# Performance work log

Hardware: AMD Instinct MI355X
Metric: run time of the kernel (lower is better)

## Reference

```python
import jax, jax.numpy as jnp
import numpy as np

D = 512
H = 8
W = 128  # window_size
HD = D // H
EPS = 1e-5


def _layernorm(x, g, b):
    mu = jnp.mean(x, axis=-1, keepdims=True)
    var = jnp.mean(jnp.square(x - mu), axis=-1, keepdims=True)
    return (x - mu) * jax.lax.rsqrt(var + EPS) * g + b


def setup_inputs() -> dict:
    key = jax.random.key(0)
    ks = jax.random.split(key, 6)
    B, S = 4, 8192
    src = jax.random.normal(ks[0], (B, S, D), jnp.float32)
    sc = 1.0 / np.sqrt(D)
    in_proj_w = jax.random.normal(ks[1], (3 * D, D), jnp.float32) * sc
    in_proj_b = jnp.zeros((3 * D,), jnp.float32)
    out_w = jax.random.normal(ks[2], (D, D), jnp.float32) * sc
    out_b = jnp.zeros((D,), jnp.float32)
    w1 = jax.random.normal(ks[3], (4 * D, D), jnp.float32) * sc
    b1 = jnp.zeros((4 * D,), jnp.float32)
    w2 = jax.random.normal(ks[4], (D, 4 * D), jnp.float32) * (1.0 / np.sqrt(4 * D))
    b2 = jnp.zeros((D,), jnp.float32)
    return {
        'src': src,
        'in_proj_w': in_proj_w, 'in_proj_b': in_proj_b,
        'out_w': out_w, 'out_b': out_b,
        'ln1_g': jnp.ones((D,), jnp.float32), 'ln1_b': jnp.zeros((D,), jnp.float32),
        'w1': w1, 'b1': b1, 'w2': w2, 'b2': b2,
        'ln2_g': jnp.ones((D,), jnp.float32), 'ln2_b': jnp.zeros((D,), jnp.float32),
    }


def reference(src, in_proj_w, in_proj_b, out_w, out_b, ln1_g, ln1_b,
              w1, b1, w2, b2, ln2_g, ln2_b):
    B, S, _ = src.shape
    nW = S // W
    x = src.reshape(B, nW, W, D)  # block-diagonal windows
    # packed qkv projection (torch MultiheadAttention in_proj)
    qkv = jnp.einsum('bnwd,ed->bnwe', x, in_proj_w) + in_proj_b
    q, k, v = jnp.split(qkv, 3, axis=-1)
    q = q.reshape(B, nW, W, H, HD)
    k = k.reshape(B, nW, W, H, HD)
    v = v.reshape(B, nW, W, H, HD)
    scores = jnp.einsum('bnqhd,bnkhd->bnhqk', q, k) / np.sqrt(HD)
    probs = jax.nn.softmax(scores, axis=-1)
    attn = jnp.einsum('bnhqk,bnkhd->bnqhd', probs, v).reshape(B, nW, W, D)
    attn = jnp.einsum('bnwd,ed->bnwe', attn, out_w) + out_b
    x = _layernorm(x + attn, ln1_g, ln1_b)
    ff = jnp.einsum('bnwf,df->bnwd', jax.nn.relu(jnp.einsum('bnwd,fd->bnwf', x, w1) + b1), w2) + b2
    x = _layernorm(x + ff, ln2_g, ln2_b)
    return x.reshape(B, S, D)
```

## Files before the change

### kernel.cpp

```cpp
#include <hip/hip_runtime.h>
#include <hip/hip_bf16.h>
#include <math.h>

typedef __bf16 bf16;
typedef bf16 bf16x8 __attribute__((ext_vector_type(8)));
typedef bf16 bf16x4 __attribute__((ext_vector_type(4)));
typedef float f32x4 __attribute__((ext_vector_type(4)));

#define MFMA16(a, b, c) __builtin_amdgcn_mfma_f32_16x16x32_bf16(a, b, c, 0, 0, 0)

__device__ __forceinline__ uint32_t swz(uint32_t base, uint32_t row, uint32_t rs, uint32_t cb) {
    return base + row * rs + (((cb >> 4) ^ (row & 7u)) << 4) + (cb & 15u);
}

__device__ __forceinline__ void gload16(const void* g, void* l) {
    __builtin_amdgcn_global_load_lds((const __attribute__((address_space(1))) void*)g,
                                     (__attribute__((address_space(3))) void*)l, 16, 0, 0);
}



__global__ void wcvt_kernel(const float* __restrict__ wqkv, const float* __restrict__ wout,
                            const float* __restrict__ w1f, const float* __restrict__ w2f,
                            bf16* __restrict__ o) {
    int i = blockIdx.x * blockDim.x + threadIdx.x;
    const float* s;
    int soff, doff;
    if (i < 98304) {
        int u = i;
        int tile = u >> 10, c = (u >> 8) & 3, nn = u & 255;
        int n = (tile >> 4) * 256 + nn;
        int k = (tile & 15) * 32 + c * 8;
        s = wqkv; soff = n * 512 + k; doff = u * 8;
    } else if (i < 131072) {
        int u = i - 98304;
        int tile = u >> 11, c = (u >> 9) & 3, nn = u & 511;
        int k = tile * 32 + c * 8;
        s = wout; soff = nn * 512 + k; doff = 786432 + u * 8;
    } else if (i < 262144) {
        int u = i - 131072;
        int tile = u >> 10, c = (u >> 8) & 3, nn = u & 255;
        int n = (tile >> 4) * 256 + nn;
        int k = (tile & 15) * 32 + c * 8;
        s = w1f; soff = n * 512 + k; doff = 1048576 + u * 8;
    } else {
        int u = i - 262144;
        int tile = u >> 10, c = (u >> 8) & 3, nn = u & 255;
        int n = (tile >> 6) * 256 + nn;
        int k = (tile & 63) * 32 + c * 8;
        s = w2f; soff = n * 2048 + k; doff = 2097152 + u * 8;
    }
    float4 v0 = *(const float4*)(s + soff);
    float4 v1 = *(const float4*)(s + soff + 4);
    bf16x8 h = { (bf16)v0.x, (bf16)v0.y, (bf16)v0.z, (bf16)v0.w,
                 (bf16)v1.x, (bf16)v1.y, (bf16)v1.z, (bf16)v1.w };
    *(bf16x8*)(o + doff) = h;
}

__global__ void xcvt_kernel(float* __restrict__ src) {
    int row = blockIdx.x * 4 + (threadIdx.x >> 6);
    int l = threadIdx.x & 63;
    float* rp = src + (size_t)row * 512 + l * 8;
    float4 v0 = *(const float4*)rp;
    float4 v1 = *(const float4*)(rp + 4);
    asm volatile("s_waitcnt vmcnt(0)" ::: "memory");
    bf16x8 h = { (bf16)v0.x, (bf16)v0.y, (bf16)v0.z, (bf16)v0.w,
                 (bf16)v1.x, (bf16)v1.y, (bf16)v1.z, (bf16)v1.w };
    *(bf16x8*)((bf16*)(src + (size_t)row * 512) + l * 8) = h;
}

#define N256_LOOP(NT)                                                                  \
    int ib = 0;                                                                        \
    _Pragma("unroll 1")                                                                \
    for (int t = 0; t < (NT); ++t) {                                                   \
        int in2 = ib + 2; if (in2 >= 3) in2 -= 3;                                      \
        const uint32_t A0 = (uint32_t)ib * 8192u;                                      \
        const uint32_t B0 = 24576u + (uint32_t)ib * 16384u;                            \
        bf16x8 a[4], b[4];                                                             \
        _Pragma("unroll")                                                              \
        for (int i = 0; i < 4; ++i)                                                    \
            a[i] = *(const bf16x8*)(smem + A0 + quad * 2048 + (wm * 64 + i * 16 + l16) * 16); \
        _Pragma("unroll")                                                              \
        for (int nt = 0; nt < 4; ++nt)                                                 \
            b[nt] = *(const bf16x8*)(smem + B0 + quad * 4096 + (wn * 64 + nt * 16 + l16) * 16); \
        if (t + 2 < (NT)) { STAGE_A(in2, t + 2); STAGE_B2(in2, t + 2, 0); STAGE_B2(in2, t + 2, 1); } \
        _Pragma("unroll")                                                              \
        for (int nt = 0; nt < 4; ++nt)                                                 \
            _Pragma("unroll")                                                          \
            for (int i = 0; i < 4; ++i) acc[i][nt] = MFMA16(a[i], b[nt], acc[i][nt]);  \
        if (t + 2 < (NT)) asm volatile("s_waitcnt vmcnt(3)" ::: "memory");             \
        else              asm volatile("s_waitcnt vmcnt(0)" ::: "memory");             \
        __builtin_amdgcn_s_barrier();                                                  \
        ib = (ib == 2) ? 0 : ib + 1;                                                   \
    }

#define PHASED_LOOP(NT)                                                                \
    int ib = 0;                                                                        \
    _Pragma("unroll 1")                                                                \
    for (int t = 0; t < (NT); ++t) {                                                   \
        int in2 = ib + 2; if (in2 >= 3) in2 -= 3;                                      \
        const uint32_t A0 = (uint32_t)ib * 8192u;                                      \
        const uint32_t B0 = 24576u + (uint32_t)ib * 32768u;                            \
        bf16x8 a[4], b[8];                                                             \
                                                                \
        _Pragma("unroll")                                                              \
        for (int i = 0; i < 4; ++i)                                                    \
            a[i] = *(const bf16x8*)(smem + A0 + quad * 2048 + (wm * 64 + i * 16 + l16) * 16); \
        _Pragma("unroll")                                                              \
        for (int nt = 0; nt < 4; ++nt)                                                 \
            b[nt] = *(const bf16x8*)(smem + B0 + quad * 8192 + (wn * 128 + nt * 16 + l16) * 16); \
        if (t + 2 < (NT)) { STAGE_A(in2, t + 2); STAGE_B(in2, t + 2, 0); }             \
        __builtin_amdgcn_s_barrier();                                                  \
        asm volatile("s_waitcnt lgkmcnt(0)" ::: "memory");                             \
        __builtin_amdgcn_sched_barrier(0);                                             \
        __builtin_amdgcn_s_setprio(1);                                                 \
        _Pragma("unroll")                                                              \
        for (int nt = 0; nt < 4; ++nt)                                                 \
            _Pragma("unroll")                                                          \
            for (int i = 0; i < 4; ++i) acc[i][nt] = MFMA16(a[i], b[nt], acc[i][nt]);  \
        __builtin_amdgcn_s_setprio(0);                                                 \
        __builtin_amdgcn_s_barrier();                                                  \
                                                                \
        _Pragma("unroll")                                                              \
        for (int nt = 4; nt < 8; ++nt)                                                 \
            b[nt] = *(const bf16x8*)(smem + B0 + quad * 8192 + (wn * 128 + nt * 16 + l16) * 16); \
        if (t + 2 < (NT)) { STAGE_B(in2, t + 2, 1); STAGE_B(in2, t + 2, 2); STAGE_B(in2, t + 2, 3); } \
        __builtin_amdgcn_s_barrier();                                                  \
        asm volatile("s_waitcnt lgkmcnt(0)" ::: "memory");                             \
        __builtin_amdgcn_sched_barrier(0);                                             \
        __builtin_amdgcn_s_setprio(1);                                                 \
        _Pragma("unroll")                                                              \
        for (int nt = 4; nt < 8; ++nt)                                                 \
            _Pragma("unroll")                                                          \
            for (int i = 0; i < 4; ++i) acc[i][nt] = MFMA16(a[i], b[nt], acc[i][nt]);  \
        __builtin_amdgcn_s_setprio(0);                                                 \
        if (t + 2 < (NT)) asm volatile("s_waitcnt vmcnt(5)" ::: "memory");             \
        else              asm volatile("s_waitcnt vmcnt(0)" ::: "memory");             \
        __builtin_amdgcn_s_barrier();                                                  \
        ib = (ib == 2) ? 0 : ib + 1;                                                   \
    }

extern "C" __global__ __launch_bounds__(512, 4)
void qkv_kernel(const char* __restrict__ xb, const char* __restrict__ Wqkvp,
                const float* __restrict__ bqkv, char* __restrict__ qOb,
                char* __restrict__ kvb) {
    extern __shared__ char smem[];
    const int tid = threadIdx.x;
    const int w = tid >> 6, lane = tid & 63, l16 = lane & 15, quad = lane >> 4;
    const int wm = w >> 2, wn = w & 3;
    const int mb = blockIdx.x, cb = blockIdx.y;

    f32x4 acc[4][4];
#pragma unroll
    for (int i = 0; i < 4; ++i)
#pragma unroll
        for (int nt = 0; nt < 4; ++nt) acc[i][nt] = (f32x4){0.f, 0.f, 0.f, 0.f};

#define STAGE_A(ib_, t_)                                                               \
    {                                                                                  \
        int ca = w >> 1, rg = w & 1;                                                   \
        gload16(xb + (size_t)(mb * 128 + rg * 64 + lane) * 2048 + (t_) * 64 + ca * 16, \
                smem + (uint32_t)(ib_) * 8192u + ca * 2048 + rg * 1024);               \
    }
#define STAGE_B2(ib_, t_, j_)                                                          \
    {                                                                                  \
        int idx = w * 2 + (j_), c = idx >> 2, ng = idx & 3;                            \
        gload16(Wqkvp + (size_t)(cb * 16 + (t_)) * 16384 + c * 4096 + ng * 1024 + lane * 16, \
                smem + 24576u + (uint32_t)(ib_) * 16384u + (uint32_t)c * 4096 + (uint32_t)ng * 1024); \
    }

    STAGE_A(0, 0); STAGE_B2(0, 0, 0); STAGE_B2(0, 0, 1);
    STAGE_A(1, 1); STAGE_B2(1, 1, 0); STAGE_B2(1, 1, 1);
    asm volatile("s_waitcnt vmcnt(3)" ::: "memory");
    __builtin_amdgcn_s_barrier();

    N256_LOOP(16)
#undef STAGE_A
#undef STAGE_B2

    const uint32_t sb = 24576u + (uint32_t)w * 2048u;
#pragma unroll
    for (int i = 0; i < 4; ++i) {
#pragma unroll
        for (int nt = 0; nt < 4; ++nt) {
            float bb = bqkv[cb * 256 + wn * 64 + nt * 16 + l16];
#pragma unroll
            for (int r = 0; r < 4; ++r)
                *(bf16*)(smem + swz(sb, quad * 4 + r, 128, (nt * 16 + l16) * 2)) =
                    (bf16)(acc[i][nt][r] + bb);
        }
        asm volatile("s_waitcnt lgkmcnt(0)" ::: "memory");
#pragma unroll
        for (int t2 = 0; t2 < 2; ++t2) {
            int row = t2 * 8 + (lane >> 3), ch = lane & 7;
            bf16x8 v = *(bf16x8*)(smem + swz(sb, row, 128, ch * 16));
            size_t row_g = (size_t)(mb * 128 + wm * 64 + i * 16 + row);
            int cbyte = wn * 128 + ch * 16;
            if (cb < 2)      *(bf16x8*)(qOb + row_g * 1024 + cb * 512 + cbyte) = v;
            else if (cb < 4) *(bf16x8*)(kvb + row_g * 2048 + (cb - 2) * 512 + cbyte) = v;
            else             *(bf16x8*)(kvb + row_g * 2048 + 1024 + (cb - 4) * 512 + cbyte) = v;
        }
        asm volatile("s_waitcnt lgkmcnt(0)" ::: "memory");
    }
}

#define AVT 0u
#define ASCR 16384u
extern "C" __global__ __launch_bounds__(512, 4)
void attn_kernel(char* __restrict__ qOb, const char* __restrict__ kvb) {
    extern __shared__ char smem[];
    const int tid = threadIdx.x;
    const int wid = tid >> 6, lane = tid & 63, l16 = lane & 15, quad = lane >> 4;
    const int win = blockIdx.x >> 3, head = blockIdx.x & 7;
    const size_t wrow0 = (size_t)win * 128;
    f32x4 zero4 = { 0.f, 0.f, 0.f, 0.f };

    {
        int key = tid >> 2, d0 = (tid & 3) * 16;
        const char* vs = kvb + (wrow0 + key) * 2048 + 1024 + head * 128 + d0 * 2;
#pragma unroll
        for (int j = 0; j < 2; ++j) {
            bf16x8 v = *(const bf16x8*)(vs + j * 16);
#pragma unroll
            for (int e = 0; e < 8; ++e)
                *(bf16*)(smem + swz(AVT, d0 + j * 8 + e, 256, key * 2)) = v[e];
        }
    }
    __syncthreads();

    bf16x8 qf[2];
#pragma unroll
    for (int ks = 0; ks < 2; ++ks)
        qf[ks] = *(const bf16x8*)(qOb + (wrow0 + wid * 16 + l16) * 1024 + head * 128 + ks * 64 + quad * 16);

    f32x4 sa[8];
#pragma unroll
    for (int nt = 0; nt < 8; ++nt) sa[nt] = zero4;
#pragma unroll
    for (int nt = 0; nt < 8; ++nt)
#pragma unroll
        for (int ks = 0; ks < 2; ++ks) {
            bf16x8 kb = *(const bf16x8*)(kvb + (wrow0 + nt * 16 + l16) * 2048 + head * 128 + ks * 64 + quad * 16);
            sa[nt] = MFMA16(qf[ks], kb, sa[nt]);
        }
#pragma unroll
    for (int nt = 0; nt < 8; ++nt) sa[nt] *= 0.125f;
#pragma unroll
    for (int r = 0; r < 4; ++r) {
        float m = sa[0][r];
#pragma unroll
        for (int nt = 1; nt < 8; ++nt) m = fmaxf(m, sa[nt][r]);
#pragma unroll
        for (int sft = 1; sft < 16; sft <<= 1) m = fmaxf(m, __shfl_xor(m, sft, 64));
        float s = 0.f;
#pragma unroll
        for (int nt = 0; nt < 8; ++nt) {
            float e = __expf(sa[nt][r] - m);
            sa[nt][r] = e;
            s += e;
        }
#pragma unroll
        for (int sft = 1; sft < 16; sft <<= 1) s += __shfl_xor(s, sft, 64);
        float inv = 1.0f / s;
#pragma unroll
        for (int nt = 0; nt < 8; ++nt) sa[nt][r] *= inv;
    }

    const uint32_t sb = ASCR + (uint32_t)wid * 2048;
    bf16x8 pf[4];
#pragma unroll
    for (int hf = 0; hf < 2; ++hf) {
#pragma unroll
        for (int nt = 0; nt < 4; ++nt)
#pragma unroll
            for (int r = 0; r < 4; ++r)
                *(bf16*)(smem + swz(sb, quad * 4 + r, 128, (nt * 16 + l16) * 2)) = (bf16)sa[hf * 4 + nt][r];
        asm volatile("s_waitcnt lgkmcnt(0)" ::: "memory");
#pragma unroll
        for (int ks = 0; ks < 2; ++ks)
            pf[hf * 2 + ks] = *(bf16x8*)(smem + swz(sb, l16, 128, ks * 64 + quad * 16));
        asm volatile("s_waitcnt lgkmcnt(0)" ::: "memory");
    }

    f32x4 ov[4];
#pragma unroll
    for (int nt = 0; nt < 4; ++nt) {
        ov[nt] = zero4;
#pragma unroll
        for (int ks = 0; ks < 4; ++ks) {
            bf16x8 vb = *(bf16x8*)(smem + swz(AVT, nt * 16 + l16, 256, ks * 64 + quad * 16));
            ov[nt] = MFMA16(pf[ks], vb, ov[nt]);
        }
    }
#pragma unroll
    for (int hf = 0; hf < 2; ++hf) {
#pragma unroll
        for (int nt = 0; nt < 2; ++nt)
#pragma unroll
            for (int r = 0; r < 4; ++r)
                *(bf16*)(smem + swz(sb, quad * 4 + r, 128, (nt * 16 + l16) * 2)) = (bf16)ov[hf * 2 + nt][r];
        asm volatile("s_waitcnt lgkmcnt(0)" ::: "memory");
        {
            int row = lane >> 2, ch = lane & 3;
            bf16x8 v = *(bf16x8*)(smem + swz(sb, row, 128, ch * 16));
            *(bf16x8*)(qOb + (wrow0 + wid * 16 + row) * 1024 + head * 128 + hf * 64 + ch * 16) = v;
        }
        asm volatile("s_waitcnt lgkmcnt(0)" ::: "memory");
    }
}

extern "C" __global__ __launch_bounds__(512, 2)
void outproj_kernel(char* __restrict__ srcb, const char* __restrict__ qOb,
                    const char* __restrict__ Woutp, const float* __restrict__ bout,
                    const float* __restrict__ g1, const float* __restrict__ be1) {
    extern __shared__ char smem[];
    const int tid = threadIdx.x;
    const int w = tid >> 6, lane = tid & 63, l16 = lane & 15, quad = lane >> 4;
    const int wm = w >> 2, wn = w & 3;
    const int mb = blockIdx.x;

    f32x4 acc[4][8];
#pragma unroll
    for (int i = 0; i < 4; ++i)
#pragma unroll
        for (int nt = 0; nt < 8; ++nt) acc[i][nt] = (f32x4){0.f, 0.f, 0.f, 0.f};

#define STAGE_A(ib_, t_)                                                               \
    {                                                                                  \
        int ca = w >> 1, rg = w & 1;                                                   \
        gload16(qOb + (size_t)(mb * 128 + rg * 64 + lane) * 1024 + (t_) * 64 + ca * 16, \
                smem + (uint32_t)(ib_) * 8192u + ca * 2048 + rg * 1024);               \
    }
#define STAGE_B(ib_, t_, j_)                                                           \
    {                                                                                  \
        int idx = w * 4 + (j_), c = idx >> 3, ng = idx & 7;                            \
        gload16(Woutp + (size_t)(t_) * 32768 + c * 8192 + ng * 1024 + lane * 16,       \
                smem + 24576u + (uint32_t)(ib_) * 32768u + (uint32_t)c * 8192 + (uint32_t)ng * 1024); \
    }

    STAGE_A(0, 0); STAGE_B(0, 0, 0); STAGE_B(0, 0, 1); STAGE_B(0, 0, 2); STAGE_B(0, 0, 3);
    STAGE_A(1, 1); STAGE_B(1, 1, 0); STAGE_B(1, 1, 1); STAGE_B(1, 1, 2); STAGE_B(1, 1, 3);
    asm volatile("s_waitcnt vmcnt(5)" ::: "memory");
    __builtin_amdgcn_s_barrier();

    PHASED_LOOP(16)
#undef STAGE_A
#undef STAGE_B

#pragma unroll
    for (int nt = 0; nt < 8; ++nt) {
        int col = wn * 128 + nt * 16 + l16;
        float bb = bout[col];
#pragma unroll
        for (int i = 0; i < 4; ++i)
#pragma unroll
            for (int r = 0; r < 4; ++r) {
                int row = mb * 128 + wm * 64 + i * 16 + quad * 4 + r;
                float xv = (float)*(const bf16*)(srcb + (size_t)row * 2048 + col * 2);
                acc[i][nt][r] += bb + xv;
            }
    }
    float ps[4][4], ps2[4][4];
#pragma unroll
    for (int i = 0; i < 4; ++i)
#pragma unroll
        for (int r = 0; r < 4; ++r) {
            float s = 0.f, s2 = 0.f;
#pragma unroll
            for (int nt = 0; nt < 8; ++nt) {
                float v = acc[i][nt][r];
                s += v;
                s2 += v * v;
            }
#pragma unroll
            for (int sft = 1; sft < 16; sft <<= 1) {
                s += __shfl_xor(s, sft, 64);
                s2 += __shfl_xor(s2, sft, 64);
            }
            ps[i][r] = s;
            ps2[i][r] = s2;
        }
    if (l16 == 0) {
#pragma unroll
        for (int i = 0; i < 4; ++i)
#pragma unroll
            for (int r = 0; r < 4; ++r) {
                int row_l = wm * 64 + i * 16 + quad * 4 + r;
                *(float*)(smem + row_l * 32 + wn * 8) = ps[i][r];
                *(float*)(smem + row_l * 32 + wn * 8 + 4) = ps2[i][r];
            }
    }
    __syncthreads();
    const uint32_t sb = 24576u + (uint32_t)w * 4096u;
#pragma unroll
    for (int i = 0; i < 4; ++i) {
#pragma unroll
        for (int r = 0; r < 4; ++r) {
            int row_l = wm * 64 + i * 16 + quad * 4 + r;
            float S = 0.f, S2 = 0.f;
#pragma unroll
            for (int w4 = 0; w4 < 4; ++w4) {
                S += *(const float*)(smem + row_l * 32 + w4 * 8);
                S2 += *(const float*)(smem + row_l * 32 + w4 * 8 + 4);
            }
            float mu = S * (1.0f / 512.0f);
            float var = S2 * (1.0f / 512.0f) - mu * mu;
            float rstd = rsqrtf(var + 1e-5f);
#pragma unroll
            for (int nt = 0; nt < 8; ++nt) {
                int col = wn * 128 + nt * 16 + l16;
                float v = (acc[i][nt][r] - mu) * rstd * g1[col] + be1[col];
                *(bf16*)(smem + swz(sb, quad * 4 + r, 256, (nt * 16 + l16) * 2)) = (bf16)v;
            }
        }
        asm volatile("s_waitcnt lgkmcnt(0)" ::: "memory");
#pragma unroll
        for (int j = 0; j < 4; ++j) {
            int uu = j * 64 + lane;
            int row = uu >> 4, ch = uu & 15;
            bf16x8 v = *(bf16x8*)(smem + swz(sb, row, 256, ch * 16));
            *(bf16x8*)(srcb + (size_t)(mb * 128 + wm * 64 + i * 16 + row) * 2048 + 1024 +
                       wn * 256 + ch * 16) = v;
        }
        asm volatile("s_waitcnt lgkmcnt(0)" ::: "memory");
    }
}

extern "C" __global__ __launch_bounds__(512, 4)
void ff1_kernel(char* __restrict__ srcb, const char* __restrict__ W1p,
                const float* __restrict__ b1, char* __restrict__ doutb,
                char* __restrict__ wsOb) {
    extern __shared__ char smem[];
    const int tid = threadIdx.x;
    const int w = tid >> 6, lane = tid & 63, l16 = lane & 15, quad = lane >> 4;
    const int wm = w >> 2, wn = w & 3;
    const int mb = blockIdx.x, cb = blockIdx.y;

    f32x4 acc[4][4];
#pragma unroll
    for (int i = 0; i < 4; ++i)
#pragma unroll
        for (int nt = 0; nt < 4; ++nt) acc[i][nt] = (f32x4){0.f, 0.f, 0.f, 0.f};

#define STAGE_A(ib_, t_)                                                               \
    {                                                                                  \
        int ca = w >> 1, rg = w & 1;                                                   \
        gload16(srcb + (size_t)(mb * 128 + rg * 64 + lane) * 2048 + 1024 + (t_) * 64 + ca * 16, \
                smem + (uint32_t)(ib_) * 8192u + ca * 2048 + rg * 1024);               \
    }
#define STAGE_B2(ib_, t_, j_)                                                          \
    {                                                                                  \
        int idx = w * 2 + (j_), c = idx >> 2, ng = idx & 3;                            \
        gload16(W1p + (size_t)(cb * 16 + (t_)) * 16384 + c * 4096 + ng * 1024 + lane * 16, \
                smem + 24576u + (uint32_t)(ib_) * 16384u + (uint32_t)c * 4096 + (uint32_t)ng * 1024); \
    }

    STAGE_A(0, 0); STAGE_B2(0, 0, 0); STAGE_B2(0, 0, 1);
    STAGE_A(1, 1); STAGE_B2(1, 1, 0); STAGE_B2(1, 1, 1);
    asm volatile("s_waitcnt vmcnt(3)" ::: "memory");
    __builtin_amdgcn_s_barrier();

    N256_LOOP(16)
#undef STAGE_A
#undef STAGE_B2

    const uint32_t sb = 24576u + (uint32_t)w * 2048u;
#pragma unroll
    for (int i = 0; i < 4; ++i) {
#pragma unroll
        for (int nt = 0; nt < 4; ++nt) {
            float bb = b1[cb * 256 + wn * 64 + nt * 16 + l16];
#pragma unroll
            for (int r = 0; r < 4; ++r)
                *(bf16*)(smem + swz(sb, quad * 4 + r, 128, (nt * 16 + l16) * 2)) =
                    (bf16)fmaxf(acc[i][nt][r] + bb, 0.0f);
        }
        asm volatile("s_waitcnt lgkmcnt(0)" ::: "memory");
#pragma unroll
        for (int t2 = 0; t2 < 2; ++t2) {
            int row = t2 * 8 + (lane >> 3), ch = lane & 7;
            bf16x8 v = *(bf16x8*)(smem + swz(sb, row, 128, ch * 16));
            size_t row_g = (size_t)(mb * 128 + wm * 64 + i * 16 + row);
            int cbyte = wn * 128 + ch * 16;
            if (cb < 4)      *(bf16x8*)(doutb + row_g * 2048 + cb * 512 + cbyte) = v;
            else if (cb < 6) *(bf16x8*)(srcb + row_g * 2048 + (cb - 4) * 512 + cbyte) = v;
            else             *(bf16x8*)(wsOb + row_g * 1024 + (cb - 6) * 512 + cbyte) = v;
        }
        asm volatile("s_waitcnt lgkmcnt(0)" ::: "memory");
    }
}

extern "C" __global__ __launch_bounds__(512, 4)
void ff2_kernel(char* __restrict__ doutb, const char* __restrict__ srcb,
                const char* __restrict__ wsOb, const char* __restrict__ W2p,
                const float* __restrict__ b2) {
    extern __shared__ char smem[];
    const int tid = threadIdx.x;
    const int w = tid >> 6, lane = tid & 63, l16 = lane & 15, quad = lane >> 4;
    const int wm = w >> 2, wn = w & 3;
    const int mb = blockIdx.x, cb = blockIdx.y;

    f32x4 acc[4][4];
#pragma unroll
    for (int i = 0; i < 4; ++i)
#pragma unroll
        for (int nt = 0; nt < 4; ++nt) acc[i][nt] = (f32x4){0.f, 0.f, 0.f, 0.f};

#define STAGE_A(ib_, t_)                                                               \
    {                                                                                  \
        const char* hb; int rstride, koffb;                                            \
        if ((t_) < 32)      { hb = doutb; rstride = 2048; koffb = (t_) * 64; }         \
        else if ((t_) < 48) { hb = srcb;  rstride = 2048; koffb = ((t_) - 32) * 64; }  \
        else                { hb = wsOb;  rstride = 1024; koffb = ((t_) - 48) * 64; }  \
        int ca = w >> 1, rg = w & 1;                                                   \
        gload16(hb + (size_t)(mb * 128 + rg * 64 + lane) * rstride + koffb + ca * 16,  \
                smem + (uint32_t)(ib_) * 8192u + ca * 2048 + rg * 1024);               \
    }
#define STAGE_B2(ib_, t_, j_)                                                          \
    {                                                                                  \
        int idx = w * 2 + (j_), c = idx >> 2, ng = idx & 3;                            \
        gload16(W2p + (size_t)(cb * 64 + (t_)) * 16384 + c * 4096 + ng * 1024 + lane * 16, \
                smem + 24576u + (uint32_t)(ib_) * 16384u + (uint32_t)c * 4096 + (uint32_t)ng * 1024); \
    }

    STAGE_A(0, 0); STAGE_B2(0, 0, 0); STAGE_B2(0, 0, 1);
    STAGE_A(1, 1); STAGE_B2(1, 1, 0); STAGE_B2(1, 1, 1);
    asm volatile("s_waitcnt vmcnt(3)" ::: "memory");
    __builtin_amdgcn_s_barrier();

    N256_LOOP(64)
#undef STAGE_A
#undef STAGE_B2

#pragma unroll
    for (int nt = 0; nt < 4; ++nt) {
        int col = cb * 256 + wn * 64 + nt * 16 + l16;
        float bb = b2[col];
#pragma unroll
        for (int i = 0; i < 4; ++i)
#pragma unroll
            for (int r = 0; r < 4; ++r) {
                int row = mb * 128 + wm * 64 + i * 16 + quad * 4 + r;
                float x1v = (float)*(const bf16*)(srcb + (size_t)row * 2048 + 1024 + col * 2);
                *(float*)(doutb + (size_t)row * 2048 + col * 4) = acc[i][nt][r] + bb + x1v;
            }
    }
}

extern "C" __global__ __launch_bounds__(256)
void ln2_kernel(float* __restrict__ y, const float* __restrict__ g2,
                const float* __restrict__ be2) {
    int row = blockIdx.x * 4 + (threadIdx.x >> 6);
    int lane = threadIdx.x & 63;
    float* rp = y + (size_t)row * 512 + lane * 8;
    float4 v0 = *(const float4*)rp;
    float4 v1 = *(const float4*)(rp + 4);
    float s = v0.x + v0.y + v0.z + v0.w + v1.x + v1.y + v1.z + v1.w;
    float s2 = v0.x * v0.x + v0.y * v0.y + v0.z * v0.z + v0.w * v0.w +
               v1.x * v1.x + v1.y * v1.y + v1.z * v1.z + v1.w * v1.w;
#pragma unroll
    for (int sft = 1; sft < 64; sft <<= 1) {
        s += __shfl_xor(s, sft, 64);
        s2 += __shfl_xor(s2, sft, 64);
    }
    float mu = s * (1.0f / 512.0f);
    float var = s2 * (1.0f / 512.0f) - mu * mu;
    float rstd = rsqrtf(var + 1e-5f);
    const float* gp = g2 + lane * 8;
    const float* bp = be2 + lane * 8;
    float4 o0, o1;
    o0.x = (v0.x - mu) * rstd * gp[0] + bp[0];
    o0.y = (v0.y - mu) * rstd * gp[1] + bp[1];
    o0.z = (v0.z - mu) * rstd * gp[2] + bp[2];
    o0.w = (v0.w - mu) * rstd * gp[3] + bp[3];
    o1.x = (v1.x - mu) * rstd * gp[4] + bp[4];
    o1.y = (v1.y - mu) * rstd * gp[5] + bp[5];
    o1.z = (v1.z - mu) * rstd * gp[6] + bp[6];
    o1.w = (v1.w - mu) * rstd * gp[7] + bp[7];
    *(float4*)rp = o0;
    *(float4*)(rp + 4) = o1;
}

extern "C" void kernel_launch(void* const* d_in, const int* in_sizes, int n_in,
                              void* d_out, int out_size, void* d_ws, size_t ws_size,
                              hipStream_t stream) {
    (void)in_sizes; (void)n_in; (void)out_size; (void)ws_size;
    float* src = (float*)d_in[0];
    const float* ipw = (const float*)d_in[1];
    const float* ipb = (const float*)d_in[2];
    const float* ow  = (const float*)d_in[3];
    const float* ob  = (const float*)d_in[4];
    const float* g1  = (const float*)d_in[5];
    const float* be1 = (const float*)d_in[6];
    const float* w1  = (const float*)d_in[7];
    const float* b1  = (const float*)d_in[8];
    const float* w2  = (const float*)d_in[9];
    const float* b2  = (const float*)d_in[10];
    const float* g2  = (const float*)d_in[11];
    const float* be2 = (const float*)d_in[12];
    bf16* ws = (bf16*)d_ws;
    char* srcb = (char*)src;
    char* doutb = (char*)d_out;
    char* qOb = (char*)d_ws + 6291456;

    wcvt_kernel<<<1536, 256, 0, stream>>>(ipw, ow, w1, w2, ws);
    xcvt_kernel<<<8192, 256, 0, stream>>>(src);

    hipFuncSetAttribute((const void*)qkv_kernel, hipFuncAttributeMaxDynamicSharedMemorySize, 73728);
    hipFuncSetAttribute((const void*)attn_kernel, hipFuncAttributeMaxDynamicSharedMemorySize, 32768);
    hipFuncSetAttribute((const void*)outproj_kernel, hipFuncAttributeMaxDynamicSharedMemorySize, 122880);
    hipFuncSetAttribute((const void*)ff1_kernel, hipFuncAttributeMaxDynamicSharedMemorySize, 73728);
    hipFuncSetAttribute((const void*)ff2_kernel, hipFuncAttributeMaxDynamicSharedMemorySize, 73728);

    qkv_kernel<<<dim3(256, 6), 512, 73728, stream>>>(srcb, (const char*)ws, ipb, qOb, doutb);
    attn_kernel<<<2048, 512, 32768, stream>>>(qOb, doutb);
    outproj_kernel<<<256, 512, 122880, stream>>>(srcb, qOb, (const char*)(ws + 786432), ob, g1, be1);
    ff1_kernel<<<dim3(256, 8), 512, 73728, stream>>>(srcb, (const char*)(ws + 1048576), b1, doutb, qOb);
    ff2_kernel<<<dim3(256, 2), 512, 73728, stream>>>(doutb, srcb, qOb, (const char*)(ws + 2097152), b2);
    ln2_kernel<<<8192, 256, 0, stream>>>((float*)doutb, g2, be2);
}
```

Measured before the change: 488.6 us.

## Switch GEMMs to double-buffered LDS and split outproj with separate LN1 kernel

The shared GEMM loop goes from triple-buffered to double-buffered LDS, prefetching only one tile ahead and waiting on all loads each iteration. This cuts dynamic shared memory from 72KB to 48KB per block to allow more resident blocks. The out-projection is split over two 256-column blocks using the common N256 loop instead of the phased 512-wide loop, writing fp32 pre-norm output to a buffer. A new row-wise ln1_kernel then applies LayerNorm1, which adds a kernel launch and an extra fp32 round trip through global memory. The trade is less latency hiding in the main loop in exchange for higher occupancy and simpler code.

```diff
diff --git a/kernel.cpp b/kernel.cpp
--- a/kernel.cpp
+++ b/kernel.cpp
@@ -34,9 +34,10 @@
         s = wqkv; soff = n * 512 + k; doff = u * 8;
     } else if (i < 131072) {
         int u = i - 98304;
-        int tile = u >> 11, c = (u >> 9) & 3, nn = u & 511;
-        int k = tile * 32 + c * 8;
-        s = wout; soff = nn * 512 + k; doff = 786432 + u * 8;
+        int tile = u >> 10, c = (u >> 8) & 3, nn = u & 255;
+        int n = (tile >> 4) * 256 + nn;
+        int k = (tile & 15) * 32 + c * 8;
+        s = wout; soff = n * 512 + k; doff = 786432 + u * 8;
     } else if (i < 262144) {
         int u = i - 131072;
         int tile = u >> 10, c = (u >> 8) & 3, nn = u & 255;
@@ -73,9 +74,9 @@
     int ib = 0;                                                                        \
     _Pragma("unroll 1")                                                                \
     for (int t = 0; t < (NT); ++t) {                                                   \
-        int in2 = ib + 2; if (in2 >= 3) in2 -= 3;                                      \
+        if (t + 1 < (NT)) { STAGE_A(ib ^ 1, t + 1); STAGE_B2(ib ^ 1, t + 1, 0); STAGE_B2(ib ^ 1, t + 1, 1); } \
         const uint32_t A0 = (uint32_t)ib * 8192u;                                      \
-        const uint32_t B0 = 24576u + (uint32_t)ib * 16384u;                            \
+        const uint32_t B0 = 16384u + (uint32_t)ib * 16384u;                            \
         bf16x8 a[4], b[4];                                                             \
         _Pragma("unroll")                                                              \
         for (int i = 0; i < 4; ++i)                                                    \
@@ -83,61 +84,13 @@
         _Pragma("unroll")                                                              \
         for (int nt = 0; nt < 4; ++nt)                                                 \
             b[nt] = *(const bf16x8*)(smem + B0 + quad * 4096 + (wn * 64 + nt * 16 + l16) * 16); \
-        if (t + 2 < (NT)) { STAGE_A(in2, t + 2); STAGE_B2(in2, t + 2, 0); STAGE_B2(in2, t + 2, 1); } \
         _Pragma("unroll")                                                              \
         for (int nt = 0; nt < 4; ++nt)                                                 \
             _Pragma("unroll")                                                          \
             for (int i = 0; i < 4; ++i) acc[i][nt] = MFMA16(a[i], b[nt], acc[i][nt]);  \
-        if (t + 2 < (NT)) asm volatile("s_waitcnt vmcnt(3)" ::: "memory");             \
-        else              asm volatile("s_waitcnt vmcnt(0)" ::: "memory");             \
+        asm volatile("s_waitcnt vmcnt(0)" ::: "memory");                               \
         __builtin_amdgcn_s_barrier();                                                  \
-        ib = (ib == 2) ? 0 : ib + 1;                                                   \
-    }
-
-#define PHASED_LOOP(NT)                                                                \
-    int ib = 0;                                                                        \
-    _Pragma("unroll 1")                                                                \
-    for (int t = 0; t < (NT); ++t) {                                                   \
-        int in2 = ib + 2; if (in2 >= 3) in2 -= 3;                                      \
-        const uint32_t A0 = (uint32_t)ib * 8192u;                                      \
-        const uint32_t B0 = 24576u + (uint32_t)ib * 32768u;                            \
-        bf16x8 a[4], b[8];                                                             \
-                                                                \
-        _Pragma("unroll")                                                              \
-        for (int i = 0; i < 4; ++i)                                                    \
-            a[i] = *(const bf16x8*)(smem + A0 + quad * 2048 + (wm * 64 + i * 16 + l16) * 16); \
-        _Pragma("unroll")                                                              \
-        for (int nt = 0; nt < 4; ++nt)                                                 \
-            b[nt] = *(const bf16x8*)(smem + B0 + quad * 8192 + (wn * 128 + nt * 16 + l16) * 16); \
-        if (t + 2 < (NT)) { STAGE_A(in2, t + 2); STAGE_B(in2, t + 2, 0); }             \
-        __builtin_amdgcn_s_barrier();                                                  \
-        asm volatile("s_waitcnt lgkmcnt(0)" ::: "memory");                             \
-        __builtin_amdgcn_sched_barrier(0);                                             \
-        __builtin_amdgcn_s_setprio(1);                                                 \
-        _Pragma("unroll")                                                              \
-        for (int nt = 0; nt < 4; ++nt)                                                 \
-            _Pragma("unroll")                                                          \
-            for (int i = 0; i < 4; ++i) acc[i][nt] = MFMA16(a[i], b[nt], acc[i][nt]);  \
-        __builtin_amdgcn_s_setprio(0);                                                 \
-        __builtin_amdgcn_s_barrier();                                                  \
-                                                                \
-        _Pragma("unroll")                                                              \
-        for (int nt = 4; nt < 8; ++nt)                                                 \
-            b[nt] = *(const bf16x8*)(smem + B0 + quad * 8192 + (wn * 128 + nt * 16 + l16) * 16); \
-        if (t + 2 < (NT)) { STAGE_B(in2, t + 2, 1); STAGE_B(in2, t + 2, 2); STAGE_B(in2, t + 2, 3); } \
-        __builtin_amdgcn_s_barrier();                                                  \
-        asm volatile("s_waitcnt lgkmcnt(0)" ::: "memory");                             \
-        __builtin_amdgcn_sched_barrier(0);                                             \
-        __builtin_amdgcn_s_setprio(1);                                                 \
-        _Pragma("unroll")                                                              \
-        for (int nt = 4; nt < 8; ++nt)                                                 \
-            _Pragma("unroll")                                                          \
-            for (int i = 0; i < 4; ++i) acc[i][nt] = MFMA16(a[i], b[nt], acc[i][nt]);  \
-        __builtin_amdgcn_s_setprio(0);                                                 \
-        if (t + 2 < (NT)) asm volatile("s_waitcnt vmcnt(5)" ::: "memory");             \
-        else              asm volatile("s_waitcnt vmcnt(0)" ::: "memory");             \
-        __builtin_amdgcn_s_barrier();                                                  \
-        ib = (ib == 2) ? 0 : ib + 1;                                                   \
+        ib ^= 1;                                                                       \
     }
 
 extern "C" __global__ __launch_bounds__(512, 4)
@@ -166,19 +119,18 @@
     {                                                                                  \
         int idx = w * 2 + (j_), c = idx >> 2, ng = idx & 3;                            \
         gload16(Wqkvp + (size_t)(cb * 16 + (t_)) * 16384 + c * 4096 + ng * 1024 + lane * 16, \
-                smem + 24576u + (uint32_t)(ib_) * 16384u + (uint32_t)c * 4096 + (uint32_t)ng * 1024); \
+                smem + 16384u + (uint32_t)(ib_) * 16384u + (uint32_t)c * 4096 + (uint32_t)ng * 1024); \
     }
 
     STAGE_A(0, 0); STAGE_B2(0, 0, 0); STAGE_B2(0, 0, 1);
-    STAGE_A(1, 1); STAGE_B2(1, 1, 0); STAGE_B2(1, 1, 1);
-    asm volatile("s_waitcnt vmcnt(3)" ::: "memory");
+    asm volatile("s_waitcnt vmcnt(0)" ::: "memory");
     __builtin_amdgcn_s_barrier();
 
     N256_LOOP(16)
 #undef STAGE_A
 #undef STAGE_B2
 
-    const uint32_t sb = 24576u + (uint32_t)w * 2048u;
+    const uint32_t sb = 16384u + (uint32_t)w * 2048u;
 #pragma unroll
     for (int i = 0; i < 4; ++i) {
 #pragma unroll
@@ -309,21 +261,21 @@
     }
 }
 
-extern "C" __global__ __launch_bounds__(512, 2)
-void outproj_kernel(char* __restrict__ srcb, const char* __restrict__ qOb,
+extern "C" __global__ __launch_bounds__(512, 4)
+void outproj_kernel(const char* __restrict__ srcb, const char* __restrict__ qOb,
                     const char* __restrict__ Woutp, const float* __restrict__ bout,
-                    const float* __restrict__ g1, const float* __restrict__ be1) {
+                    char* __restrict__ doutb) {
     extern __shared__ char smem[];
     const int tid = threadIdx.x;
     const int w = tid >> 6, lane = tid & 63, l16 = lane & 15, quad = lane >> 4;
     const int wm = w >> 2, wn = w & 3;
-    const int mb = blockIdx.x;
-
-    f32x4 acc[4][8];
+    const int mb = blockIdx.x, cb = blockIdx.y;
+
+    f32x4 acc[4][4];
 #pragma unroll
     for (int i = 0; i < 4; ++i)
 #pragma unroll
-        for (int nt = 0; nt < 8; ++nt) acc[i][nt] = (f32x4){0.f, 0.f, 0.f, 0.f};
+        for (int nt = 0; nt < 4; ++nt) acc[i][nt] = (f32x4){0.f, 0.f, 0.f, 0.f};
 
 #define STAGE_A(ib_, t_)                                                               \
     {                                                                                  \
@@ -331,25 +283,24 @@
         gload16(qOb + (size_t)(mb * 128 + rg * 64 + lane) * 1024 + (t_) * 64 + ca * 16, \
                 smem + (uint32_t)(ib_) * 8192u + ca * 2048 + rg * 1024);               \
     }
-#define STAGE_B(ib_, t_, j_)                                                           \
-    {                                                                                  \
-        int idx = w * 4 + (j_), c = idx >> 3, ng = idx & 7;                            \
-        gload16(Woutp + (size_t)(t_) * 32768 + c * 8192 + ng * 1024 + lane * 16,       \
-                smem + 24576u + (uint32_t)(ib_) * 32768u + (uint32_t)c * 8192 + (uint32_t)ng * 1024); \
-    }
-
-    STAGE_A(0, 0); STAGE_B(0, 0, 0); STAGE_B(0, 0, 1); STAGE_B(0, 0, 2); STAGE_B(0, 0, 3);
-    STAGE_A(1, 1); STAGE_B(1, 1, 0); STAGE_B(1, 1, 1); STAGE_B(1, 1, 2); STAGE_B(1, 1, 3);
-    asm volatile("s_waitcnt vmcnt(5)" ::: "memory");
+#define STAGE_B2(ib_, t_, j_)                                                          \
+    {                                                                                  \
+        int idx = w * 2 + (j_), c = idx >> 2, ng = idx & 3;                            \
+        gload16(Woutp + (size_t)(cb * 16 + (t_)) * 16384 + c * 4096 + ng * 1024 + lane * 16, \
+                smem + 16384u + (uint32_t)(ib_) * 16384u + (uint32_t)c * 4096 + (uint32_t)ng * 1024); \
+    }
+
+    STAGE_A(0, 0); STAGE_B2(0, 0, 0); STAGE_B2(0, 0, 1);
+    asm volatile("s_waitcnt vmcnt(0)" ::: "memory");
     __builtin_amdgcn_s_barrier();
 
-    PHASED_LOOP(16)
+    N256_LOOP(16)
 #undef STAGE_A
-#undef STAGE_B
-
-#pragma unroll
-    for (int nt = 0; nt < 8; ++nt) {
-        int col = wn * 128 + nt * 16 + l16;
+#undef STAGE_B2
+
+#pragma unroll
+    for (int nt = 0; nt < 4; ++nt) {
+        int col = cb * 256 + wn * 64 + nt * 16 + l16;
         float bb = bout[col];
 #pragma unroll
         for (int i = 0; i < 4; ++i)
@@ -357,73 +308,42 @@
             for (int r = 0; r < 4; ++r) {
                 int row = mb * 128 + wm * 64 + i * 16 + quad * 4 + r;
                 float xv = (float)*(const bf16*)(srcb + (size_t)row * 2048 + col * 2);
-                acc[i][nt][r] += bb + xv;
+                *(float*)(doutb + (size_t)row * 2048 + col * 4) = acc[i][nt][r] + bb + xv;
             }
     }
-    float ps[4][4], ps2[4][4];
-#pragma unroll
-    for (int i = 0; i < 4; ++i)
-#pragma unroll
-        for (int r = 0; r < 4; ++r) {
-            float s = 0.f, s2 = 0.f;
-#pragma unroll
-            for (int nt = 0; nt < 8; ++nt) {
-                float v = acc[i][nt][r];
-                s += v;
-                s2 += v * v;
-            }
-#pragma unroll
-            for (int sft = 1; sft < 16; sft <<= 1) {
-                s += __shfl_xor(s, sft, 64);
-                s2 += __shfl_xor(s2, sft, 64);
-            }
-            ps[i][r] = s;
-            ps2[i][r] = s2;
-        }
-    if (l16 == 0) {
-#pragma unroll
-        for (int i = 0; i < 4; ++i)
-#pragma unroll
-            for (int r = 0; r < 4; ++r) {
-                int row_l = wm * 64 + i * 16 + quad * 4 + r;
-                *(float*)(smem + row_l * 32 + wn * 8) = ps[i][r];
-                *(float*)(smem + row_l * 32 + wn * 8 + 4) = ps2[i][r];
-            }
-    }
-    __syncthreads();
-    const uint32_t sb = 24576u + (uint32_t)w * 4096u;
-#pragma unroll
-    for (int i = 0; i < 4; ++i) {
-#pragma unroll
-        for (int r = 0; r < 4; ++r) {
-            int row_l = wm * 64 + i * 16 + quad * 4 + r;
-            float S = 0.f, S2 = 0.f;
-#pragma unroll
-            for (int w4 = 0; w4 < 4; ++w4) {
-                S += *(const float*)(smem + row_l * 32 + w4 * 8);
-                S2 += *(const float*)(smem + row_l * 32 + w4 * 8 + 4);
-            }
-            float mu = S * (1.0f / 512.0f);
-            float var = S2 * (1.0f / 512.0f) - mu * mu;
-            float rstd = rsqrtf(var + 1e-5f);
-#pragma unroll
-            for (int nt = 0; nt < 8; ++nt) {
-                int col = wn * 128 + nt * 16 + l16;
-                float v = (acc[i][nt][r] - mu) * rstd * g1[col] + be1[col];
-                *(bf16*)(smem + swz(sb, quad * 4 + r, 256, (nt * 16 + l16) * 2)) = (bf16)v;
-            }
-        }
-        asm volatile("s_waitcnt lgkmcnt(0)" ::: "memory");
-#pragma unroll
-        for (int j = 0; j < 4; ++j) {
-            int uu = j * 64 + lane;
-            int row = uu >> 4, ch = uu & 15;
-            bf16x8 v = *(bf16x8*)(smem + swz(sb, row, 256, ch * 16));
-            *(bf16x8*)(srcb + (size_t)(mb * 128 + wm * 64 + i * 16 + row) * 2048 + 1024 +
-                       wn * 256 + ch * 16) = v;
-        }
-        asm volatile("s_waitcnt lgkmcnt(0)" ::: "memory");
-    }
+}
+
+extern "C" __global__ __launch_bounds__(256)
+void ln1_kernel(const float* __restrict__ y1, char* __restrict__ srcb,
+                const float* __restrict__ g1, const float* __restrict__ be1) {
+    int row = blockIdx.x * 4 + (threadIdx.x >> 6);
+    int lane = threadIdx.x & 63;
+    const float* rp = y1 + (size_t)row * 512 + lane * 8;
+    float4 v0 = *(const float4*)rp;
+    float4 v1 = *(const float4*)(rp + 4);
+    float s = v0.x + v0.y + v0.z + v0.w + v1.x + v1.y + v1.z + v1.w;
+    float s2 = v0.x * v0.x + v0.y * v0.y + v0.z * v0.z + v0.w * v0.w +
+               v1.x * v1.x + v1.y * v1.y + v1.z * v1.z + v1.w * v1.w;
+#pragma unroll
+    for (int sft = 1; sft < 64; sft <<= 1) {
+        s += __shfl_xor(s, sft, 64);
+        s2 += __shfl_xor(s2, sft, 64);
+    }
+    float mu = s * (1.0f / 512.0f);
+    float var = s2 * (1.0f / 512.0f) - mu * mu;
+    float rstd = rsqrtf(var + 1e-5f);
+    const float* gp = g1 + lane * 8;
+    const float* bp = be1 + lane * 8;
+    bf16x8 h;
+    h[0] = (bf16)((v0.x - mu) * rstd * gp[0] + bp[0]);
+    h[1] = (bf16)((v0.y - mu) * rstd * gp[1] + bp[1]);
+    h[2] = (bf16)((v0.z - mu) * rstd * gp[2] + bp[2]);
+    h[3] = (bf16)((v0.w - mu) * rstd * gp[3] + bp[3]);
+    h[4] = (bf16)((v1.x - mu) * rstd * gp[4] + bp[4]);
+    h[5] = (bf16)((v1.y - mu) * rstd * gp[5] + bp[5]);
+    h[6] = (bf16)((v1.z - mu) * rstd * gp[6] + bp[6]);
+    h[7] = (bf16)((v1.w - mu) * rstd * gp[7] + bp[7]);
+    *(bf16x8*)(srcb + (size_t)row * 2048 + 1024 + lane * 16) = h;
 }
 
 extern "C" __global__ __launch_bounds__(512, 4)
@@ -452,19 +372,18 @@
     {                                                                                  \
         int idx = w * 2 + (j_), c = idx >> 2, ng = idx & 3;                            \
         gload16(W1p + (size_t)(cb * 16 + (t_)) * 16384 + c * 4096 + ng * 1024 + lane * 16, \
-                smem + 24576u + (uint32_t)(ib_) * 16384u + (uint32_t)c * 4096 + (uint32_t)ng * 1024); \
+                smem + 16384u + (uint32_t)(ib_) * 16384u + (uint32_t)c * 4096 + (uint32_t)ng * 1024); \
     }
 
     STAGE_A(0, 0); STAGE_B2(0, 0, 0); STAGE_B2(0, 0, 1);
-    STAGE_A(1, 1); STAGE_B2(1, 1, 0); STAGE_B2(1, 1, 1);
-    asm volatile("s_waitcnt vmcnt(3)" ::: "memory");
+    asm volatile("s_waitcnt vmcnt(0)" ::: "memory");
     __builtin_amdgcn_s_barrier();
 
     N256_LOOP(16)
 #undef STAGE_A
 #undef STAGE_B2
 
-    const uint32_t sb = 24576u + (uint32_t)w * 2048u;
+    const uint32_t sb = 16384u + (uint32_t)w * 2048u;
 #pragma unroll
     for (int i = 0; i < 4; ++i) {
 #pragma unroll
@@ -520,12 +439,11 @@
     {                                                                                  \
         int idx = w * 2 + (j_), c = idx >> 2, ng = idx & 3;                            \
         gload16(W2p + (size_t)(cb * 64 + (t_)) * 16384 + c * 4096 + ng * 1024 + lane * 16, \
-                smem + 24576u + (uint32_t)(ib_) * 16384u + (uint32_t)c * 4096 + (uint32_t)ng * 1024); \
+                smem + 16384u + (uint32_t)(ib_) * 16384u + (uint32_t)c * 4096 + (uint32_t)ng * 1024); \
     }
 
     STAGE_A(0, 0); STAGE_B2(0, 0, 0); STAGE_B2(0, 0, 1);
-    STAGE_A(1, 1); STAGE_B2(1, 1, 0); STAGE_B2(1, 1, 1);
-    asm volatile("s_waitcnt vmcnt(3)" ::: "memory");
+    asm volatile("s_waitcnt vmcnt(0)" ::: "memory");
     __builtin_amdgcn_s_barrier();
 
     N256_LOOP(64)
@@ -606,16 +524,17 @@
     wcvt_kernel<<<1536, 256, 0, stream>>>(ipw, ow, w1, w2, ws);
     xcvt_kernel<<<8192, 256, 0, stream>>>(src);
 
-    hipFuncSetAttribute((const void*)qkv_kernel, hipFuncAttributeMaxDynamicSharedMemorySize, 73728);
+    hipFuncSetAttribute((const void*)qkv_kernel, hipFuncAttributeMaxDynamicSharedMemorySize, 49152);
     hipFuncSetAttribute((const void*)attn_kernel, hipFuncAttributeMaxDynamicSharedMemorySize, 32768);
-    hipFuncSetAttribute((const void*)outproj_kernel, hipFuncAttributeMaxDynamicSharedMemorySize, 122880);
-    hipFuncSetAttribute((const void*)ff1_kernel, hipFuncAttributeMaxDynamicSharedMemorySize, 73728);
-    hipFuncSetAttribute((const void*)ff2_kernel, hipFuncAttributeMaxDynamicSharedMemorySize, 73728);
-
-    qkv_kernel<<<dim3(256, 6), 512, 73728, stream>>>(srcb, (const char*)ws, ipb, qOb, doutb);
+    hipFuncSetAttribute((const void*)outproj_kernel, hipFuncAttributeMaxDynamicSharedMemorySize, 49152);
+    hipFuncSetAttribute((const void*)ff1_kernel, hipFuncAttributeMaxDynamicSharedMemorySize, 49152);
+    hipFuncSetAttribute((const void*)ff2_kernel, hipFuncAttributeMaxDynamicSharedMemorySize, 49152);
+
+    qkv_kernel<<<dim3(256, 6), 512, 49152, stream>>>(srcb, (const char*)ws, ipb, qOb, doutb);
     attn_kernel<<<2048, 512, 32768, stream>>>(qOb, doutb);
-    outproj_kernel<<<256, 512, 122880, stream>>>(srcb, qOb, (const char*)(ws + 786432), ob, g1, be1);
-    ff1_kernel<<<dim3(256, 8), 512, 73728, stream>>>(srcb, (const char*)(ws + 1048576), b1, doutb, qOb);
-    ff2_kernel<<<dim3(256, 2), 512, 73728, stream>>>(doutb, srcb, qOb, (const char*)(ws + 2097152), b2);
+    outproj_kernel<<<dim3(256, 2), 512, 49152, stream>>>(srcb, qOb, (const char*)(ws + 786432), ob, doutb);
+    ln1_kernel<<<8192, 256, 0, stream>>>((const float*)doutb, srcb, g1, be1);
+    ff1_kernel<<<dim3(256, 8), 512, 49152, stream>>>(srcb, (const char*)(ws + 1048576), b1, doutb, qOb);
+    ff2_kernel<<<dim3(256, 2), 512, 49152, stream>>>(doutb, srcb, qOb, (const char*)(ws + 2097152), b2);
     ln2_kernel<<<8192, 256, 0, stream>>>((float*)doutb, g2, be2);
 }
```

Result: slower. 501.0 us (+2.5%).
